# Optimization experiments

Hardware: AMD Instinct MI355X
Metric: run time of the kernel (lower is better)

## Reference

```python
import jax, jax.numpy as jnp
import numpy as np

MASK_VALUE = -10000000.0


def setup_inputs() -> dict:
    key = jax.random.key(0)
    ks = jax.random.split(key, 8)
    U, I, J, C, E = 128, 256, 512, 128, 128
    return {
        "target_items_context": jax.random.normal(ks[0], (U, I, C), jnp.float32),
        "interacted_items_context": jax.random.normal(ks[1], (U, J, C), jnp.float32),
        "user_embeds": jax.random.normal(ks[2], (U, E), jnp.float32),
        "attention_mask": jax.random.randint(ks[3], (U, J), 0, 2) > 0,
        "w_dense": jax.random.normal(ks[4], (2 * C,), jnp.float32) * 0.02,
        "b_dense": jax.random.normal(ks[5], (1,), jnp.float32) * 0.02,
        "W_mlp": jax.random.normal(ks[6], (E + C, C), jnp.float32) * 0.02,
        "b_mlp": jax.random.normal(ks[7], (C,), jnp.float32) * 0.02,
    }


def reference(target_items_context, interacted_items_context, user_embeds,
              attention_mask, w_dense, b_dense, W_mlp, b_mlp):
    C = target_items_context.shape[-1]
    E = user_embeds.shape[-1]
    # additive attention score: tanh([t; k] @ w + b) = tanh(t@w1 + k@w2 + b)
    # (dropout is identity in eval mode)
    s_t = jnp.einsum('uic,c->ui', target_items_context, w_dense[:C])      # (U, I)
    s_k = jnp.einsum('ujc,c->uj', interacted_items_context, w_dense[C:])  # (U, J)
    scores = jnp.tanh(s_t[:, :, None] + s_k[:, None, :] + b_dense[0])     # (U, I, J)
    scores = scores + (~attention_mask)[:, None, :].astype(scores.dtype) * MASK_VALUE
    attn = jax.nn.softmax(scores, axis=-1)                                # (U, I, J)
    # weighted pooling of interacted contexts
    pooled = jnp.einsum('uij,ujc->uic', attn, interacted_items_context)   # (U, I, C)
    # mlp: relu([user; pooled] @ W + b) = relu(user@W[:E] + pooled@W[E:] + b)
    u_part = user_embeds @ W_mlp[:E]                                      # (U, C)
    user_context = jax.nn.relu(u_part[:, None, :] + pooled @ W_mlp[E:] + b_mlp)
    return user_context, attn
```

## Files before the change

kernel.cpp:

```cpp
#include <hip/hip_runtime.h>

#define UU 128
#define II 256
#define JJ 512
#define CC 128
#define EE 128
#define IB 16
#define NIB 16
#define JT 64
#define NJT 8
#define VTP 72

typedef short bf16x8 __attribute__((ext_vector_type(8)));
typedef float f32x4 __attribute__((ext_vector_type(4)));

union FragU { bf16x8 v; unsigned u[4]; };

__device__ __forceinline__ float fast_tanh(float x) {
    float ex = __expf(2.0f * x);
    return 1.0f - 2.0f / (ex + 1.0f);
}

__device__ __forceinline__ unsigned pack_bf16x2(float lo, float hi) {
    unsigned ul = __float_as_uint(lo), uh = __float_as_uint(hi);
    ul = (ul + 0x7FFFu + ((ul >> 16) & 1u)) >> 16;
    uh = (uh + 0x7FFFu + ((uh >> 16) & 1u)) >> 16;
    return ul | (uh << 16);
}

__device__ __forceinline__ short bf16s(float f) {
    unsigned u = __float_as_uint(f);
    u = (u + 0x7FFFu + ((u >> 16) & 1u)) >> 16;
    return (short)u;
}

__device__ __forceinline__ float wave_reduce_add(float v) {
#pragma unroll
    for (int k = 32; k >= 1; k >>= 1) v += __shfl_xor(v, k, 64);
    return v;
}

#define ST_BLOCKS (UU * II / 4)
#define UP_BLOCKS (UU * CC / 256)
#define VT_BLOCKS (UU * NJT)

__global__ void precompute_kernel(const float* __restrict__ tgt,
                                  const float* __restrict__ itc,
                                  const float* __restrict__ user,
                                  const float* __restrict__ wd,
                                  const float* __restrict__ bd,
                                  const float* __restrict__ Wm,
                                  const float* __restrict__ bm,
                                  float* __restrict__ st_g,
                                  float* __restrict__ sk_g,
                                  float* __restrict__ up_g,
                                  short* __restrict__ vtg,
                                  short* __restrict__ wtg) {
    __shared__ float vt_f[JT][CC + 4];
    int b = blockIdx.x;
    int t = threadIdx.x;
    if (b < ST_BLOCKS) {
        int row = b * 4 + (t >> 6);
        int lane = t & 63;
        float2 a = *(const float2*)&tgt[(size_t)row * CC + lane * 2];
        float2 w = *(const float2*)&wd[lane * 2];
        float s = wave_reduce_add(a.x * w.x + a.y * w.y);
        if (lane == 0) st_g[row] = s + bd[0];
    } else if (b < ST_BLOCKS + UP_BLOCKS) {
        int idx = (b - ST_BLOCKS) * 256 + t;
        int u = idx >> 7, c = idx & 127;
        float acc = bm[c];
#pragma unroll 8
        for (int e = 0; e < EE; ++e) acc += user[u * EE + e] * Wm[e * CC + c];
        up_g[idx] = acc;
    } else if (b < ST_BLOCKS + UP_BLOCKS + VT_BLOCKS) {
        int vb = b - ST_BLOCKS - UP_BLOCKS;
        int u = vb & 127, jt = vb >> 7;
        const float* src = itc + ((size_t)u * JJ + jt * JT) * CC;
#pragma unroll
        for (int k = 0; k < 8; ++k) {
            int f = t + 256 * k;
            int row = f >> 5, c4 = (f & 31) * 4;
            *(float4*)&vt_f[row][c4] = *(const float4*)&src[(size_t)row * CC + c4];
        }
        __syncthreads();
        {
            int r = t >> 2, q4 = t & 3;
            float s = 0.f;
#pragma unroll
            for (int cc = 0; cc < 32; cc += 4) {
                float4 a = *(const float4*)&vt_f[r][q4 * 32 + cc];
                float4 w = *(const float4*)&wd[CC + q4 * 32 + cc];
                s += a.x * w.x + a.y * w.y + a.z * w.z + a.w * w.w;
            }
            s += __shfl_xor(s, 1, 64);
            s += __shfl_xor(s, 2, 64);
            if (q4 == 0) sk_g[u * JJ + jt * JT + r] = s;
        }
        {
            int c = t & 127, half = t >> 7;
            unsigned* dst = (unsigned*)(vtg + (size_t)(u * NJT + jt) * 8192) +
                            half * 2048 + c * 16;
#pragma unroll
            for (int m = 0; m < 16; ++m) {
                dst[m] = pack_bf16x2(vt_f[32 * half + 2 * m][c],
                                     vt_f[32 * half + 2 * m + 1][c]);
            }
        }
    } else {
        int n = t & 127, khalf = t >> 7;
#pragma unroll
        for (int ks2 = 0; ks2 < 2; ++ks2) {
            int ks = khalf * 2 + ks2;
#pragma unroll
            for (int g = 0; g < 4; ++g) {
                unsigned q[4];
#pragma unroll
                for (int pr = 0; pr < 4; ++pr) {
                    float lo = Wm[(size_t)(EE + 32 * ks + 8 * g + 2 * pr) * CC + n];
                    float hi = Wm[(size_t)(EE + 32 * ks + 8 * g + 2 * pr + 1) * CC + n];
                    q[pr] = pack_bf16x2(lo, hi);
                }
                *(uint4*)&wtg[ks * 4096 + n * 32 + 8 * g] =
                    make_uint4(q[0], q[1], q[2], q[3]);
            }
        }
    }
}

__global__ __launch_bounds__(256, 4) void fused_main(
    const int* __restrict__ mask, const float* __restrict__ st_g,
    const float* __restrict__ sk_g, const float* __restrict__ up_g,
    const short* __restrict__ vt_g, const short* __restrict__ wt_g,
    float* __restrict__ out_ctx, float* __restrict__ out_attn) {
    __shared__ __align__(16) short ps[8192];
    __shared__ __align__(16) short pooled_bf[2048];
    __shared__ float dinv_lds[IB];

    int b = blockIdx.x;
    int x = b & 7, qq = b >> 3;
    int u = x + 8 * (qq >> 4);
    int ib = qq & 15;
    int i0 = ib * IB;
    int t = threadIdx.x;
    int w = t >> 6, l = t & 63, ln = l & 15, g = l >> 4;

    int r = t >> 4, s4 = t & 15;
    float sv = st_g[u * II + i0 + r];
    const float* skb = sk_g + u * JJ;
    const int* mkb = mask + u * JJ;
    float pf[32];
    float rowsum = 0.f;
#pragma unroll
    for (int h = 0; h < 4; ++h) {
        int jb = 8 * (s4 + 16 * h);
        float4 k0 = *(const float4*)&skb[jb];
        float4 k1 = *(const float4*)&skb[jb + 4];
        int4 m0 = *(const int4*)&mkb[jb];
        int4 m1 = *(const int4*)&mkb[jb + 4];
        float* pp = pf + 8 * h;
        pp[0] = m0.x ? __expf(fast_tanh(sv + k0.x)) : 0.f;
        pp[1] = m0.y ? __expf(fast_tanh(sv + k0.y)) : 0.f;
        pp[2] = m0.z ? __expf(fast_tanh(sv + k0.z)) : 0.f;
        pp[3] = m0.w ? __expf(fast_tanh(sv + k0.w)) : 0.f;
        pp[4] = m1.x ? __expf(fast_tanh(sv + k1.x)) : 0.f;
        pp[5] = m1.y ? __expf(fast_tanh(sv + k1.y)) : 0.f;
        pp[6] = m1.z ? __expf(fast_tanh(sv + k1.z)) : 0.f;
        pp[7] = m1.w ? __expf(fast_tanh(sv + k1.w)) : 0.f;
        rowsum += pp[0] + pp[1] + pp[2] + pp[3] + pp[4] + pp[5] + pp[6] + pp[7];
        unsigned q0 = pack_bf16x2(pp[0], pp[1]);
        unsigned q1 = pack_bf16x2(pp[2], pp[3]);
        unsigned q2 = pack_bf16x2(pp[4], pp[5]);
        unsigned q3 = pack_bf16x2(pp[6], pp[7]);
        int gp = (s4 + 16 * h) ^ (r & 7);
        *(uint4*)((char*)ps + r * 1024 + 16 * gp) = make_uint4(q0, q1, q2, q3);
    }
    rowsum += __shfl_xor(rowsum, 1, 64);
    rowsum += __shfl_xor(rowsum, 2, 64);
    rowsum += __shfl_xor(rowsum, 4, 64);
    rowsum += __shfl_xor(rowsum, 8, 64);
    float dinv = 1.0f / rowsum;
    if (s4 == 0) dinv_lds[r] = dinv;

    {
        float* ab = out_attn + ((size_t)(u * II + i0 + r)) * JJ;
#pragma unroll
        for (int h = 0; h < 4; ++h) {
            int jb = 8 * (s4 + 16 * h);
            const float* pp = pf + 8 * h;
            *(float4*)&ab[jb] =
                make_float4(pp[0] * dinv, pp[1] * dinv, pp[2] * dinv, pp[3] * dinv);
            *(float4*)&ab[jb + 4] =
                make_float4(pp[4] * dinv, pp[5] * dinv, pp[6] * dinv, pp[7] * dinv);
        }
    }

    const short* b_base =
        vt_g + (size_t)u * (NJT * 8192) + (32 * w + ln) * 32 + 8 * g;
    bf16x8 pb0[8], pb1[8];
#pragma unroll
    for (int s = 0; s < 8; ++s) {
        int off = (s >> 1) * 8192 + (s & 1) * 4096;
        pb0[s] = *(const bf16x8*)&b_base[off];
        pb1[s] = *(const bf16x8*)&b_base[off + 512];
    }

    asm volatile("s_waitcnt lgkmcnt(0)" ::: "memory");
    __builtin_amdgcn_s_barrier();
    asm volatile("" ::: "memory");

    f32x4 acc0 = {0.f, 0.f, 0.f, 0.f};
    f32x4 acc1 = {0.f, 0.f, 0.f, 0.f};
#pragma unroll
    for (int s = 0; s < 16; ++s) {
        bf16x8 af = *(const bf16x8*)((const char*)ps + ln * 1024 +
                                     16 * ((4 * s + g) ^ (ln & 7)));
        acc0 = __builtin_amdgcn_mfma_f32_16x16x32_bf16(af, pb0[s & 7], acc0, 0, 0, 0);
        acc1 = __builtin_amdgcn_mfma_f32_16x16x32_bf16(af, pb1[s & 7], acc1, 0, 0, 0);
        if (s < 8) {
            int off = ((s + 8) >> 1) * 8192 + ((s + 8) & 1) * 4096;
            pb0[s & 7] = *(const bf16x8*)&b_base[off];
            pb1[s & 7] = *(const bf16x8*)&b_base[off + 512];
        }
    }

    const short* wbase = wt_g + (32 * w + ln) * 32 + 8 * g;
    bf16x8 wb0[4], wb1[4];
#pragma unroll
    for (int ks = 0; ks < 4; ++ks) {
        wb0[ks] = *(const bf16x8*)&wbase[ks * 4096];
        wb1[ks] = *(const bf16x8*)&wbase[ks * 4096 + 512];
    }

#pragma unroll
    for (int ri = 0; ri < 4; ++ri) {
        int row = 4 * g + ri;
        float dv = dinv_lds[row];
        int c0 = 32 * w + ln;
        int by0 = row * 256 + 16 * ((c0 >> 3) ^ (row & 7)) + 2 * (ln & 7);
        *(short*)((char*)pooled_bf + by0) = bf16s(acc0[ri] * dv);
        int c1 = c0 + 16;
        int by1 = row * 256 + 16 * ((c1 >> 3) ^ (row & 7)) + 2 * (ln & 7);
        *(short*)((char*)pooled_bf + by1) = bf16s(acc1[ri] * dv);
    }
    asm volatile("s_waitcnt lgkmcnt(0)" ::: "memory");
    __builtin_amdgcn_s_barrier();
    asm volatile("" ::: "memory");

    f32x4 oa0 = {0.f, 0.f, 0.f, 0.f};
    f32x4 oa1 = {0.f, 0.f, 0.f, 0.f};
#pragma unroll
    for (int ks = 0; ks < 4; ++ks) {
        bf16x8 pa = *(const bf16x8*)((const char*)pooled_bf + ln * 256 +
                                     16 * ((4 * ks + g) ^ (ln & 7)));
        oa0 = __builtin_amdgcn_mfma_f32_16x16x32_bf16(pa, wb0[ks], oa0, 0, 0, 0);
        oa1 = __builtin_amdgcn_mfma_f32_16x16x32_bf16(pa, wb1[ks], oa1, 0, 0, 0);
    }
    {
        int c0 = 32 * w + ln, c1 = c0 + 16;
        float up0v = up_g[u * CC + c0];
        float up1v = up_g[u * CC + c1];
        float* ctx = out_ctx + ((size_t)(u * II + i0)) * CC;
#pragma unroll
        for (int ri = 0; ri < 4; ++ri) {
            int row = 4 * g + ri;
            ctx[(size_t)row * CC + c0] = fmaxf(oa0[ri] + up0v, 0.f);
            ctx[(size_t)row * CC + c1] = fmaxf(oa1[ri] + up1v, 0.f);
        }
    }
}

__global__ __launch_bounds__(256, 3) void fused_fallback(
    const float* __restrict__ tgt, const float* __restrict__ itc,
    const float* __restrict__ user, const int* __restrict__ mask,
    const float* __restrict__ wd, const float* __restrict__ bd,
    const float* __restrict__ Wm, const float* __restrict__ bm,
    float* __restrict__ out_ctx, float* __restrict__ out_attn) {
    __shared__ __align__(16) short Vt[CC][VTP];
    __shared__ __align__(16) float pool[IB][CC + 4];
    __shared__ __align__(16) float skv[JJ];
    __shared__ __align__(16) float stv[IB];
    __shared__ __align__(16) float upv[CC];
    __shared__ __align__(16) float dinv_lds[IB];
    __shared__ unsigned char mk[JJ];

    int b = blockIdx.x;
    int x = b & 7, q = b >> 3;
    int u = x + 8 * (q >> 4);
    int ib = q & 15;
    int i0 = ib * IB;
    int t = threadIdx.x;

    mk[t] = (unsigned char)(mask[u * JJ + t] != 0);
    mk[t + 256] = (unsigned char)(mask[u * JJ + t + 256] != 0);

    {
        int lane = t & 63, w4 = t >> 6;
        float2 w2 = *(const float2*)&wd[CC + lane * 2];
        for (int r = w4; r < JJ; r += 4) {
            float2 a = *(const float2*)&itc[((size_t)u * JJ + r) * CC + lane * 2];
            float s = wave_reduce_add(a.x * w2.x + a.y * w2.y);
            if (lane == 0) skv[r] = s;
        }
        float2 w1 = *(const float2*)&wd[lane * 2];
        float bdv = bd[0];
        for (int r = w4; r < IB; r += 4) {
            float2 a = *(const float2*)&tgt[((size_t)u * II + i0 + r) * CC + lane * 2];
            float s = wave_reduce_add(a.x * w1.x + a.y * w1.y);
            if (lane == 0) stv[r] = s + bdv;
        }
        if (t < CC) {
            float acc = bm[t];
            for (int e = 0; e < EE; ++e) acc += user[u * EE + e] * Wm[e * CC + t];
            upv[t] = acc;
        }
    }
    __syncthreads();

    const int l = t & 63;
    const int w = t >> 6;
    const int ln = l & 15;
    const int g = l >> 4;

    bf16x8 a[16];
    float rowsum = 0.0f;
    {
        float s = stv[ln];
#pragma unroll
        for (int t16 = 0; t16 < 16; ++t16) {
            int j = 32 * t16 + 8 * g;
            float4 k0 = *(const float4*)&skv[j];
            float4 k1 = *(const float4*)&skv[j + 4];
            unsigned m0 = *(const unsigned*)&mk[j];
            unsigned m1 = *(const unsigned*)&mk[j + 4];
            float pf[8];
            pf[0] = (m0 & 0x000000FFu) ? __expf(fast_tanh(s + k0.x)) : 0.0f;
            pf[1] = (m0 & 0x0000FF00u) ? __expf(fast_tanh(s + k0.y)) : 0.0f;
            pf[2] = (m0 & 0x00FF0000u) ? __expf(fast_tanh(s + k0.z)) : 0.0f;
            pf[3] = (m0 & 0xFF000000u) ? __expf(fast_tanh(s + k0.w)) : 0.0f;
            pf[4] = (m1 & 0x000000FFu) ? __expf(fast_tanh(s + k1.x)) : 0.0f;
            pf[5] = (m1 & 0x0000FF00u) ? __expf(fast_tanh(s + k1.y)) : 0.0f;
            pf[6] = (m1 & 0x00FF0000u) ? __expf(fast_tanh(s + k1.z)) : 0.0f;
            pf[7] = (m1 & 0xFF000000u) ? __expf(fast_tanh(s + k1.w)) : 0.0f;
            rowsum += pf[0] + pf[1] + pf[2] + pf[3] + pf[4] + pf[5] + pf[6] + pf[7];
            FragU cu;
            cu.u[0] = pack_bf16x2(pf[0], pf[1]);
            cu.u[1] = pack_bf16x2(pf[2], pf[3]);
            cu.u[2] = pack_bf16x2(pf[4], pf[5]);
            cu.u[3] = pack_bf16x2(pf[6], pf[7]);
            a[t16] = cu.v;
        }
    }
    rowsum += __shfl_xor(rowsum, 16, 64);
    rowsum += __shfl_xor(rowsum, 32, 64);
    float dinv = 1.0f / rowsum;
    if (t < 16) dinv_lds[t] = dinv;

    {
        float* abase = out_attn + ((size_t)(u * II + i0 + ln)) * JJ + 8 * g;
#pragma unroll
        for (int t16 = 0; t16 < 16; ++t16) {
            FragU cu; cu.v = a[t16];
            float f0 = __uint_as_float(cu.u[0] << 16) * dinv;
            float f1 = __uint_as_float(cu.u[0] & 0xFFFF0000u) * dinv;
            float f2 = __uint_as_float(cu.u[1] << 16) * dinv;
            float f3 = __uint_as_float(cu.u[1] & 0xFFFF0000u) * dinv;
            float f4 = __uint_as_float(cu.u[2] << 16) * dinv;
            float f5 = __uint_as_float(cu.u[2] & 0xFFFF0000u) * dinv;
            float f6 = __uint_as_float(cu.u[3] << 16) * dinv;
            float f7 = __uint_as_float(cu.u[3] & 0xFFFF0000u) * dinv;
            *(float4*)&abase[32 * t16] = make_float4(f0, f1, f2, f3);
            *(float4*)&abase[32 * t16 + 4] = make_float4(f4, f5, f6, f7);
        }
    }

    f32x4 acc0 = {0.f, 0.f, 0.f, 0.f};
    f32x4 acc1 = {0.f, 0.f, 0.f, 0.f};
    const float* Vu = itc + (size_t)u * JJ * CC;
    const int cg = t & 31;
    const int jp = t >> 5;
    const int n0 = w * 32;

    for (int jt = 0; jt < 8; ++jt) {
        int j0 = jt * JT;
        __syncthreads();
#pragma unroll
        for (int it = 0; it < 4; ++it) {
            int jl = 2 * (jp + 8 * it);
            const float* r0 = &Vu[(size_t)(j0 + jl) * CC];
            const float* r1 = r0 + CC;
#pragma unroll
            for (int qv = 0; qv < 4; ++qv) {
                int c = cg + 32 * qv;
                *(unsigned*)&Vt[c][jl] = pack_bf16x2(r0[c], r1[c]);
            }
        }
        __syncthreads();
#pragma unroll
        for (int kk = 0; kk < 2; ++kk) {
            bf16x8 b0 = *(const bf16x8*)&Vt[n0 + ln][32 * kk + 8 * g];
            bf16x8 b1 = *(const bf16x8*)&Vt[n0 + 16 + ln][32 * kk + 8 * g];
            acc0 = __builtin_amdgcn_mfma_f32_16x16x32_bf16(a[2 * jt + kk], b0,
                                                           acc0, 0, 0, 0);
            acc1 = __builtin_amdgcn_mfma_f32_16x16x32_bf16(a[2 * jt + kk], b1,
                                                           acc1, 0, 0, 0);
        }
    }

    __syncthreads();
    {
        float4 dv = *(const float4*)&dinv_lds[4 * g];
        float dvr[4] = {dv.x, dv.y, dv.z, dv.w};
#pragma unroll
        for (int r = 0; r < 4; ++r) {
            pool[4 * g + r][n0 + ln] = acc0[r] * dvr[r];
            pool[4 * g + r][n0 + 16 + ln] = acc1[r] * dvr[r];
        }
    }
    __syncthreads();

    {
        int tx = t & 15, ty = t >> 4;
        float o[8];
#pragma unroll
        for (int k = 0; k < 8; ++k) o[k] = 0.f;
#pragma unroll 4
        for (int k = 0; k < CC; ++k) {
            float pk = pool[ty][k];
            float4 w0 = *(const float4*)&Wm[(size_t)(EE + k) * CC + tx * 8];
            float4 w1 = *(const float4*)&Wm[(size_t)(EE + k) * CC + tx * 8 + 4];
            o[0] += pk * w0.x; o[1] += pk * w0.y; o[2] += pk * w0.z; o[3] += pk * w0.w;
            o[4] += pk * w1.x; o[5] += pk * w1.y; o[6] += pk * w1.z; o[7] += pk * w1.w;
        }
        float4 up0 = *(const float4*)&upv[tx * 8];
        float4 up1 = *(const float4*)&upv[tx * 8 + 4];
        float4 r0, r1;
        r0.x = fmaxf(o[0] + up0.x, 0.f); r0.y = fmaxf(o[1] + up0.y, 0.f);
        r0.z = fmaxf(o[2] + up0.z, 0.f); r0.w = fmaxf(o[3] + up0.w, 0.f);
        r1.x = fmaxf(o[4] + up1.x, 0.f); r1.y = fmaxf(o[5] + up1.y, 0.f);
        r1.z = fmaxf(o[6] + up1.z, 0.f); r1.w = fmaxf(o[7] + up1.w, 0.f);
        float* ctx = out_ctx + ((size_t)(u * II + i0 + ty)) * CC + tx * 8;
        *(float4*)&ctx[0] = r0;
        *(float4*)&ctx[4] = r1;
    }
}

extern "C" void kernel_launch(void* const* d_in, const int* in_sizes, int n_in,
                              void* d_out, int out_size, void* d_ws,
                              size_t ws_size, hipStream_t stream) {
    const float* tgt  = (const float*)d_in[0];
    const float* itc  = (const float*)d_in[1];
    const float* user = (const float*)d_in[2];
    const int*   mask = (const int*)d_in[3];
    const float* wd   = (const float*)d_in[4];
    const float* bd   = (const float*)d_in[5];
    const float* Wm   = (const float*)d_in[6];
    const float* bm   = (const float*)d_in[7];
    float* out_ctx  = (float*)d_out;
    float* out_attn = out_ctx + (size_t)UU * II * CC;

    size_t scalars = (size_t)(UU * II + UU * JJ + UU * CC) * sizeof(float);
    size_t vt_bytes = (size_t)UU * NJT * 8192 * sizeof(short);
    size_t wt_bytes = (size_t)16384 * sizeof(short);
    size_t need = scalars + vt_bytes + wt_bytes;
    if (ws_size >= need) {
        float* st_g = (float*)d_ws;
        float* sk_g = st_g + UU * II;
        float* up_g = sk_g + UU * JJ;
        short* vt_g = (short*)((char*)d_ws + scalars);
        short* wt_g = vt_g + (size_t)UU * NJT * 8192;
        int gridA = ST_BLOCKS + UP_BLOCKS + VT_BLOCKS + 1;
        precompute_kernel<<<gridA, 256, 0, stream>>>(
            tgt, itc, user, wd, bd, Wm, bm, st_g, sk_g, up_g, vt_g, wt_g);
        fused_main<<<UU * NIB, 256, 0, stream>>>(mask, st_g, sk_g, up_g, vt_g,
                                                 wt_g, out_ctx, out_attn);
    } else {
        fused_fallback<<<UU * NIB, 256, 0, stream>>>(
            tgt, itc, user, mask, wd, bd, Wm, bm, out_ctx, out_attn);
    }
}
```

Measured before the change: 59.53 us.

## Fuse target-score dot product into main kernel and use nontemporal output stores

Moves the per-row target score (t·w1 + b) out of the precompute kernel and into the main kernel, where each 16-thread group reads its row of the target tensor and reduces it with shuffles. This drops 8192 precompute blocks and the st_g round trip. Unnormalized probabilities are now held as packed bf16 instead of 32 floats, which cuts register pressure. The attn write is moved after the V-fragment prefetch so the two overlap. Outputs use nontemporal stores, and attn values are rebuilt from the bf16-rounded probabilities, so they lose some precision compared with fp32.

```diff
diff --git a/kernel.cpp b/kernel.cpp
--- a/kernel.cpp
+++ b/kernel.cpp
@@ -40,18 +40,14 @@
     return v;
 }
 
-#define ST_BLOCKS (UU * II / 4)
+#define VT_BLOCKS (UU * NJT)
 #define UP_BLOCKS (UU * CC / 256)
-#define VT_BLOCKS (UU * NJT)
-
-__global__ void precompute_kernel(const float* __restrict__ tgt,
-                                  const float* __restrict__ itc,
+
+__global__ void precompute_kernel(const float* __restrict__ itc,
                                   const float* __restrict__ user,
                                   const float* __restrict__ wd,
-                                  const float* __restrict__ bd,
                                   const float* __restrict__ Wm,
                                   const float* __restrict__ bm,
-                                  float* __restrict__ st_g,
                                   float* __restrict__ sk_g,
                                   float* __restrict__ up_g,
                                   short* __restrict__ vtg,
@@ -59,23 +55,8 @@
     __shared__ float vt_f[JT][CC + 4];
     int b = blockIdx.x;
     int t = threadIdx.x;
-    if (b < ST_BLOCKS) {
-        int row = b * 4 + (t >> 6);
-        int lane = t & 63;
-        float2 a = *(const float2*)&tgt[(size_t)row * CC + lane * 2];
-        float2 w = *(const float2*)&wd[lane * 2];
-        float s = wave_reduce_add(a.x * w.x + a.y * w.y);
-        if (lane == 0) st_g[row] = s + bd[0];
-    } else if (b < ST_BLOCKS + UP_BLOCKS) {
-        int idx = (b - ST_BLOCKS) * 256 + t;
-        int u = idx >> 7, c = idx & 127;
-        float acc = bm[c];
-#pragma unroll 8
-        for (int e = 0; e < EE; ++e) acc += user[u * EE + e] * Wm[e * CC + c];
-        up_g[idx] = acc;
-    } else if (b < ST_BLOCKS + UP_BLOCKS + VT_BLOCKS) {
-        int vb = b - ST_BLOCKS - UP_BLOCKS;
-        int u = vb & 127, jt = vb >> 7;
+    if (b < VT_BLOCKS) {
+        int u = b & 127, jt = b >> 7;
         const float* src = itc + ((size_t)u * JJ + jt * JT) * CC;
 #pragma unroll
         for (int k = 0; k < 8; ++k) {
@@ -107,6 +88,13 @@
                                      vt_f[32 * half + 2 * m + 1][c]);
             }
         }
+    } else if (b < VT_BLOCKS + UP_BLOCKS) {
+        int idx = (b - VT_BLOCKS) * 256 + t;
+        int u = idx >> 7, c = idx & 127;
+        float acc = bm[c];
+#pragma unroll 8
+        for (int e = 0; e < EE; ++e) acc += user[u * EE + e] * Wm[e * CC + c];
+        up_g[idx] = acc;
     } else {
         int n = t & 127, khalf = t >> 7;
 #pragma unroll
@@ -129,7 +117,8 @@
 }
 
 __global__ __launch_bounds__(256, 4) void fused_main(
-    const int* __restrict__ mask, const float* __restrict__ st_g,
+    const float* __restrict__ tgt, const int* __restrict__ mask,
+    const float* __restrict__ wd, const float* __restrict__ bd,
     const float* __restrict__ sk_g, const float* __restrict__ up_g,
     const short* __restrict__ vt_g, const short* __restrict__ wt_g,
     float* __restrict__ out_ctx, float* __restrict__ out_attn) {
@@ -144,12 +133,27 @@
     int i0 = ib * IB;
     int t = threadIdx.x;
     int w = t >> 6, l = t & 63, ln = l & 15, g = l >> 4;
-
     int r = t >> 4, s4 = t & 15;
-    float sv = st_g[u * II + i0 + r];
+
+    float sv;
+    {
+        const float* trow = tgt + ((size_t)(u * II + i0 + r)) * CC + s4 * 8;
+        float4 t0 = *(const float4*)&trow[0];
+        float4 t1 = *(const float4*)&trow[4];
+        float4 w0 = *(const float4*)&wd[s4 * 8];
+        float4 w1 = *(const float4*)&wd[s4 * 8 + 4];
+        float part = t0.x * w0.x + t0.y * w0.y + t0.z * w0.z + t0.w * w0.w +
+                     t1.x * w1.x + t1.y * w1.y + t1.z * w1.z + t1.w * w1.w;
+        part += __shfl_xor(part, 1, 64);
+        part += __shfl_xor(part, 2, 64);
+        part += __shfl_xor(part, 4, 64);
+        part += __shfl_xor(part, 8, 64);
+        sv = part + bd[0];
+    }
+
     const float* skb = sk_g + u * JJ;
     const int* mkb = mask + u * JJ;
-    float pf[32];
+    unsigned pk[16];
     float rowsum = 0.f;
 #pragma unroll
     for (int h = 0; h < 4; ++h) {
@@ -158,20 +162,21 @@
         float4 k1 = *(const float4*)&skb[jb + 4];
         int4 m0 = *(const int4*)&mkb[jb];
         int4 m1 = *(const int4*)&mkb[jb + 4];
-        float* pp = pf + 8 * h;
-        pp[0] = m0.x ? __expf(fast_tanh(sv + k0.x)) : 0.f;
-        pp[1] = m0.y ? __expf(fast_tanh(sv + k0.y)) : 0.f;
-        pp[2] = m0.z ? __expf(fast_tanh(sv + k0.z)) : 0.f;
-        pp[3] = m0.w ? __expf(fast_tanh(sv + k0.w)) : 0.f;
-        pp[4] = m1.x ? __expf(fast_tanh(sv + k1.x)) : 0.f;
-        pp[5] = m1.y ? __expf(fast_tanh(sv + k1.y)) : 0.f;
-        pp[6] = m1.z ? __expf(fast_tanh(sv + k1.z)) : 0.f;
-        pp[7] = m1.w ? __expf(fast_tanh(sv + k1.w)) : 0.f;
-        rowsum += pp[0] + pp[1] + pp[2] + pp[3] + pp[4] + pp[5] + pp[6] + pp[7];
-        unsigned q0 = pack_bf16x2(pp[0], pp[1]);
-        unsigned q1 = pack_bf16x2(pp[2], pp[3]);
-        unsigned q2 = pack_bf16x2(pp[4], pp[5]);
-        unsigned q3 = pack_bf16x2(pp[6], pp[7]);
+        float p0 = m0.x ? __expf(fast_tanh(sv + k0.x)) : 0.f;
+        float p1 = m0.y ? __expf(fast_tanh(sv + k0.y)) : 0.f;
+        float p2 = m0.z ? __expf(fast_tanh(sv + k0.z)) : 0.f;
+        float p3 = m0.w ? __expf(fast_tanh(sv + k0.w)) : 0.f;
+        float p4 = m1.x ? __expf(fast_tanh(sv + k1.x)) : 0.f;
+        float p5 = m1.y ? __expf(fast_tanh(sv + k1.y)) : 0.f;
+        float p6 = m1.z ? __expf(fast_tanh(sv + k1.z)) : 0.f;
+        float p7 = m1.w ? __expf(fast_tanh(sv + k1.w)) : 0.f;
+        rowsum += p0 + p1 + p2 + p3 + p4 + p5 + p6 + p7;
+        unsigned q0 = pack_bf16x2(p0, p1);
+        unsigned q1 = pack_bf16x2(p2, p3);
+        unsigned q2 = pack_bf16x2(p4, p5);
+        unsigned q3 = pack_bf16x2(p6, p7);
+        pk[4 * h + 0] = q0; pk[4 * h + 1] = q1;
+        pk[4 * h + 2] = q2; pk[4 * h + 3] = q3;
         int gp = (s4 + 16 * h) ^ (r & 7);
         *(uint4*)((char*)ps + r * 1024 + 16 * gp) = make_uint4(q0, q1, q2, q3);
     }
@@ -182,19 +187,6 @@
     float dinv = 1.0f / rowsum;
     if (s4 == 0) dinv_lds[r] = dinv;
 
-    {
-        float* ab = out_attn + ((size_t)(u * II + i0 + r)) * JJ;
-#pragma unroll
-        for (int h = 0; h < 4; ++h) {
-            int jb = 8 * (s4 + 16 * h);
-            const float* pp = pf + 8 * h;
-            *(float4*)&ab[jb] =
-                make_float4(pp[0] * dinv, pp[1] * dinv, pp[2] * dinv, pp[3] * dinv);
-            *(float4*)&ab[jb + 4] =
-                make_float4(pp[4] * dinv, pp[5] * dinv, pp[6] * dinv, pp[7] * dinv);
-        }
-    }
-
     const short* b_base =
         vt_g + (size_t)u * (NJT * 8192) + (32 * w + ln) * 32 + 8 * g;
     bf16x8 pb0[8], pb1[8];
@@ -203,6 +195,27 @@
         int off = (s >> 1) * 8192 + (s & 1) * 4096;
         pb0[s] = *(const bf16x8*)&b_base[off];
         pb1[s] = *(const bf16x8*)&b_base[off + 512];
+    }
+
+    {
+        float* ab = out_attn + ((size_t)(u * II + i0 + r)) * JJ;
+#pragma unroll
+        for (int h = 0; h < 4; ++h) {
+            int jb = 8 * (s4 + 16 * h);
+            unsigned q0 = pk[4 * h], q1 = pk[4 * h + 1];
+            unsigned q2 = pk[4 * h + 2], q3 = pk[4 * h + 3];
+            f32x4 v0, v1;
+            v0[0] = __uint_as_float(q0 << 16) * dinv;
+            v0[1] = __uint_as_float(q0 & 0xFFFF0000u) * dinv;
+            v0[2] = __uint_as_float(q1 << 16) * dinv;
+            v0[3] = __uint_as_float(q1 & 0xFFFF0000u) * dinv;
+            v1[0] = __uint_as_float(q2 << 16) * dinv;
+            v1[1] = __uint_as_float(q2 & 0xFFFF0000u) * dinv;
+            v1[2] = __uint_as_float(q3 << 16) * dinv;
+            v1[3] = __uint_as_float(q3 & 0xFFFF0000u) * dinv;
+            __builtin_nontemporal_store(v0, (f32x4*)&ab[jb]);
+            __builtin_nontemporal_store(v1, (f32x4*)&ab[jb + 4]);
+        }
     }
 
     asm volatile("s_waitcnt lgkmcnt(0)" ::: "memory");
@@ -264,8 +277,10 @@
 #pragma unroll
         for (int ri = 0; ri < 4; ++ri) {
             int row = 4 * g + ri;
-            ctx[(size_t)row * CC + c0] = fmaxf(oa0[ri] + up0v, 0.f);
-            ctx[(size_t)row * CC + c1] = fmaxf(oa1[ri] + up1v, 0.f);
+            __builtin_nontemporal_store(fmaxf(oa0[ri] + up0v, 0.f),
+                                        &ctx[(size_t)row * CC + c0]);
+            __builtin_nontemporal_store(fmaxf(oa1[ri] + up1v, 0.f),
+                                        &ctx[(size_t)row * CC + c1]);
         }
     }
 }
@@ -459,21 +474,20 @@
     float* out_ctx  = (float*)d_out;
     float* out_attn = out_ctx + (size_t)UU * II * CC;
 
-    size_t scalars = (size_t)(UU * II + UU * JJ + UU * CC) * sizeof(float);
+    size_t scalars = (size_t)(UU * JJ + UU * CC) * sizeof(float);
     size_t vt_bytes = (size_t)UU * NJT * 8192 * sizeof(short);
     size_t wt_bytes = (size_t)16384 * sizeof(short);
     size_t need = scalars + vt_bytes + wt_bytes;
     if (ws_size >= need) {
-        float* st_g = (float*)d_ws;
-        float* sk_g = st_g + UU * II;
+        float* sk_g = (float*)d_ws;
         float* up_g = sk_g + UU * JJ;
         short* vt_g = (short*)((char*)d_ws + scalars);
         short* wt_g = vt_g + (size_t)UU * NJT * 8192;
-        int gridA = ST_BLOCKS + UP_BLOCKS + VT_BLOCKS + 1;
-        precompute_kernel<<<gridA, 256, 0, stream>>>(
-            tgt, itc, user, wd, bd, Wm, bm, st_g, sk_g, up_g, vt_g, wt_g);
-        fused_main<<<UU * NIB, 256, 0, stream>>>(mask, st_g, sk_g, up_g, vt_g,
-                                                 wt_g, out_ctx, out_attn);
+        int gridA = VT_BLOCKS + UP_BLOCKS + 1;
+        precompute_kernel<<<gridA, 256, 0, stream>>>(itc, user, wd, Wm, bm,
+                                                     sk_g, up_g, vt_g, wt_g);
+        fused_main<<<UU * NIB, 256, 0, stream>>>(tgt, mask, wd, bd, sk_g, up_g,
+                                                 vt_g, wt_g, out_ctx, out_attn);
     } else {
         fused_fallback<<<UU * NIB, 256, 0, stream>>>(
             tgt, itc, user, mask, wd, bd, Wm, bm, out_ctx, out_attn);
```

Measured after the change: 61.18 us. 1.03x slower.
